# Performance work log

Hardware: AMD Instinct MI355X
Metric: run time of the kernel (lower is better)

## Reference

```python
import jax, jax.numpy as jnp
import numpy as np

E = 8          # num_experts
K = 2          # top_k
TEMP = 1.0     # router_temp
D = 1024       # model dim
H = 4 * D      # expert hidden dim
B, T = 2, 2048


def setup_inputs() -> dict:
    key = jax.random.key(0)
    ks = jax.random.split(key, 5)
    x = jax.random.normal(ks[0], (B, T, D), jnp.float32)
    gate_w = jax.random.normal(ks[1], (D, E), jnp.float32) * 0.02
    gate_b = jnp.zeros((E,), jnp.float32)
    w1 = jax.random.normal(ks[2], (E, D, H), jnp.float32) * 0.02
    b1 = jnp.zeros((E, H), jnp.float32)
    w2 = jax.random.normal(ks[3], (E, H, D), jnp.float32) * 0.02
    b2 = jnp.zeros((E, D), jnp.float32)
    return {"x": x, "gate_w": gate_w, "gate_b": gate_b,
            "w1": w1, "b1": b1, "w2": w2, "b2": b2}


def reference(x, gate_w, gate_b, w1, b1, w2, b2):
    b, t, d = x.shape
    xf = x.reshape(-1, d)                                    # [N, D]
    logits = xf @ gate_w + gate_b                            # [N, E]
    gates = jax.nn.softmax(logits / TEMP, axis=-1)
    topk_gates, topk_idx = jax.lax.top_k(gates, K)           # [N, K]
    topk_gates = topk_gates / (topk_gates.sum(-1, keepdims=True) + 1e-9)
    # combine weight per (token, expert): sum over k slots routed to expert e
    comb = (jax.nn.one_hot(topk_idx, E, dtype=xf.dtype)
            * topk_gates[..., None]).sum(axis=1)             # [N, E]
    out = jnp.zeros_like(xf)
    for e in range(E):  # small fixed loop over experts
        h = jax.nn.gelu(xf @ w1[e] + b1[e], approximate=False)  # exact GELU (torch default)
        out = out + comb[:, e:e + 1] * (h @ w2[e] + b2[e])
    return out.reshape(b, t, d)
```

## Files before the change

kernel.cpp:

```cpp
#include <hip/hip_runtime.h>
#include <math.h>

#define NTOK 4096
#define DIM  1024
#define HID  4096
#define NEXP 8
#define NROW 8192
#define KSPLIT 2

typedef __bf16 bf16;
typedef __attribute__((ext_vector_type(8))) __bf16 bf16x8;
typedef __attribute__((ext_vector_type(4))) float floatx4;

__device__ __forceinline__ void gl_lds16(const bf16* g, bf16* l) {
    __builtin_amdgcn_global_load_lds(
        (const __attribute__((address_space(1))) void*)g,
        (__attribute__((address_space(3))) void*)l, 16, 0, 0);
}

__device__ __forceinline__ float gelu_f(float v) {
    float x  = v * 0.70710678118654752f;
    float ax = fabsf(x);
    float t  = __builtin_amdgcn_rcpf(fmaf(0.3275911f, ax, 1.0f));
    float p  = fmaf(fmaf(fmaf(fmaf(1.061405429f, t, -1.453152027f),
                              t, 1.421413741f),
                         t, -0.284496736f),
                    t, 0.254829592f);
    p *= t;
    float ex = __expf(-x * x);
    float er = fmaf(-p, ex, 1.0f);
    er = copysignf(er, v);
    return 0.5f * v * (1.0f + er);
}

__global__ void zero_k(int* __restrict__ p) {
    if (threadIdx.x < 16) p[threadIdx.x] = 0;
}

__global__ __launch_bounds__(256) void router_k(
    const float* __restrict__ x, const float* __restrict__ gw, const float* __restrict__ gb,
    int* __restrict__ counts, int* __restrict__ tok_e, float* __restrict__ tok_g,
    bf16* __restrict__ xb)
{
    __shared__ float gws[NEXP][DIM];
    int t = threadIdx.x;
#pragma unroll
    for (int i = 0; i < 32; ++i) {
        int g = i * 256 + t;
        gws[g & 7][g >> 3] = gw[g];
    }
    __syncthreads();

    int gid = blockIdx.x * 256 + t;
    int wv = gid >> 6, lane = gid & 63;
    const float* xr = x + (size_t)wv * DIM;
    bf16* xw = xb + (size_t)wv * DIM;
    float acc[NEXP];
#pragma unroll
    for (int e = 0; e < NEXP; ++e) acc[e] = 0.f;
#pragma unroll
    for (int j = 0; j < 16; ++j) {
        int d = lane + j * 64;
        float xv = xr[d];
        xw[d] = (bf16)xv;
#pragma unroll
        for (int e = 0; e < NEXP; ++e) acc[e] += xv * gws[e][d];
    }
#pragma unroll
    for (int off = 32; off > 0; off >>= 1) {
#pragma unroll
        for (int e = 0; e < NEXP; ++e) acc[e] += __shfl_xor(acc[e], off, 64);
    }
    if (lane == 0) {
        float lg[NEXP], m = -1e30f;
        for (int e = 0; e < NEXP; ++e) { lg[e] = acc[e] + gb[e]; m = fmaxf(m, lg[e]); }
        float p[NEXP], s = 0.f;
        for (int e = 0; e < NEXP; ++e) { p[e] = expf(lg[e] - m); s += p[e]; }
        int e0 = 0;
        for (int e = 1; e < NEXP; ++e) if (p[e] > p[e0]) e0 = e;
        int e1 = (e0 == 0) ? 1 : 0;
        for (int e = 0; e < NEXP; ++e) if (e != e0 && p[e] > p[e1]) e1 = e;
        float g0 = p[e0] / s, g1 = p[e1] / s;
        float gs = g0 + g1 + 1e-9f;
        g0 /= gs; g1 /= gs;
        tok_e[wv * 2] = e0; tok_e[wv * 2 + 1] = e1;
        tok_g[wv * 2] = g0; tok_g[wv * 2 + 1] = g1;
        atomicAdd(&counts[e0], 1);
        atomicAdd(&counts[e1], 1);
    }
}

__global__ void scan_k(const int* __restrict__ counts, int* __restrict__ base)
{
    if (threadIdx.x == 0) {
        int s = 0;
#pragma unroll
        for (int e = 0; e < NEXP; ++e) { base[e] = s; s += counts[e]; }
        base[NEXP] = s;
    }
}

__global__ __launch_bounds__(256) void scatter_k(
    const int* __restrict__ tok_e, const float* __restrict__ tok_g,
    const int* __restrict__ base, int* __restrict__ counts2,
    int* __restrict__ row_token, float* __restrict__ row_gate, int* __restrict__ tok_row)
{
    int tk = blockIdx.x * 256 + threadIdx.x;
    if (tk >= NTOK) return;
#pragma unroll
    for (int k = 0; k < 2; ++k) {
        int e = tok_e[tk * 2 + k];
        int slot = atomicAdd(&counts2[e], 1);
        int r = base[e] + slot;
        row_token[r] = tk;
        row_gate[r] = tok_g[tk * 2 + k];
        tok_row[tk * 2 + k] = r;
    }
}

__global__ __launch_bounds__(256) void transpose_k(
    const float* __restrict__ src, bf16* __restrict__ dst,
    int R, int sld, size_t soff, size_t es, size_t ed)
{
    int e = blockIdx.z;
    bf16* d = dst + (size_t)e * ed;
    __shared__ __align__(16) bf16 tile[64 * 64];
    int t = threadIdx.x;
    int r0 = blockIdx.y * 64, c0 = blockIdx.x * 64;
#pragma unroll
    for (int i = 0; i < 2; ++i) {
        int c = t + i * 256;
        int rr = c >> 3, cc = c & 7;
        size_t eo = soff + (size_t)e * es + (size_t)(r0 + rr) * sld + c0 + cc * 8;
        floatx4 a = *(const floatx4*)(src + eo);
        floatx4 b = *(const floatx4*)(src + eo + 4);
        bf16x8 v;
#pragma unroll
        for (int j = 0; j < 4; ++j) { v[j] = (bf16)a[j]; v[4 + j] = (bf16)b[j]; }
        *(bf16x8*)&tile[rr * 64 + ((cc ^ ((rr >> 3) & 7)) * 8)] = v;
    }
    __syncthreads();
#pragma unroll
    for (int i = 0; i < 2; ++i) {
        int c = t + i * 256;
        int oc = c >> 3;
        int occ = c & 7;
        bf16x8 v;
#pragma unroll
        for (int j = 0; j < 8; ++j) {
            int r = occ * 8 + j;
            int p = (oc >> 3) ^ ((r >> 3) & 7);
            v[j] = tile[r * 64 + p * 8 + (oc & 7)];
        }
        *(bf16x8*)&d[(size_t)(c0 + oc) * R + r0 + occ * 8] = v;
    }
}

__global__ __launch_bounds__(256) void gemm1_k(
    const bf16* __restrict__ xb, const bf16* __restrict__ w1t, const float* __restrict__ b1,
    const int* __restrict__ counts, const int* __restrict__ base,
    const int* __restrict__ row_token, bf16* __restrict__ hbuf, int Nc, int bias_off)
{
    const int e = blockIdx.z;
    const int cnt = counts[e];
    const int rt = blockIdx.y;
    if (rt * 128 >= cnt) return;
    const int rb = base[e] + rt * 128;
    const int rend = base[e] + cnt;
    const int n0 = blockIdx.x * 128;

    __shared__ __align__(16) bf16 As[2][128 * 32];
    __shared__ __align__(16) bf16 Bs[2][128 * 32];

    const int t = threadIdx.x;
    const int wv = t >> 6, lane = t & 63;
    const int s0 = t, s1 = t + 256;
    const int ar0 = s0 >> 2, ac0 = (s0 & 3) ^ ((s0 >> 3) & 3);
    const int ar1 = s1 >> 2, ac1 = (s1 & 3) ^ ((s1 >> 3) & 3);
    int rr0 = rb + ar0; if (rr0 > NROW - 1) rr0 = NROW - 1;
    int rr1 = rb + ar1; if (rr1 > NROW - 1) rr1 = NROW - 1;
    const bf16* ga0 = xb + (size_t)row_token[rr0] * DIM + ac0 * 8;
    const bf16* ga1 = xb + (size_t)row_token[rr1] * DIM + ac1 * 8;
    const bf16* wb = w1t + (size_t)e * Nc * DIM;
    const bf16* gb0 = wb + (size_t)(n0 + ar0) * DIM + ac0 * 8;
    const bf16* gb1 = wb + (size_t)(n0 + ar1) * DIM + ac1 * 8;
    const int off0 = wv * 512, off1 = 2048 + wv * 512;

    floatx4 acc[4][4];
#pragma unroll
    for (int i = 0; i < 4; ++i)
#pragma unroll
        for (int j = 0; j < 4; ++j) acc[i][j] = floatx4{0.f, 0.f, 0.f, 0.f};

    const int wr = (wv >> 1) * 64, wc = (wv & 1) * 64;
    const int lr = lane & 15;
    const int ck = lane >> 4;

    gl_lds16(ga0, &As[0][off0]); gl_lds16(ga1, &As[0][off1]);
    gl_lds16(gb0, &Bs[0][off0]); gl_lds16(gb1, &Bs[0][off1]);

    const int NSTEP = DIM / 32;
#pragma unroll 2
    for (int i = 0; i < NSTEP; ++i) {
        const int bc = i & 1;
        asm volatile("s_waitcnt vmcnt(0)" ::: "memory");
        __builtin_amdgcn_s_barrier();
        asm volatile("" ::: "memory");
        if (i + 1 < NSTEP) {
            const int kn = (i + 1) * 32;
            gl_lds16(ga0 + kn, &As[bc ^ 1][off0]); gl_lds16(ga1 + kn, &As[bc ^ 1][off1]);
            gl_lds16(gb0 + kn, &Bs[bc ^ 1][off0]); gl_lds16(gb1 + kn, &Bs[bc ^ 1][off1]);
        }
        bf16x8 af[4], bg[4];
#pragma unroll
        for (int q = 0; q < 4; ++q) {
            int r = wr + q * 16 + lr;
            af[q] = *(const bf16x8*)&As[bc][r * 32 + ((ck ^ ((r >> 1) & 3)) * 8)];
        }
#pragma unroll
        for (int q = 0; q < 4; ++q) {
            int r = wc + q * 16 + lr;
            bg[q] = *(const bf16x8*)&Bs[bc][r * 32 + ((ck ^ ((r >> 1) & 3)) * 8)];
        }
        __builtin_amdgcn_s_setprio(1);
#pragma unroll
        for (int mi = 0; mi < 4; ++mi)
#pragma unroll
            for (int ni = 0; ni < 4; ++ni)
                acc[mi][ni] = __builtin_amdgcn_mfma_f32_16x16x32_bf16(af[mi], bg[ni], acc[mi][ni], 0, 0, 0);
        __builtin_amdgcn_s_setprio(0);
    }

#pragma unroll
    for (int mi = 0; mi < 4; ++mi) {
#pragma unroll
        for (int r = 0; r < 4; ++r) {
            int m = wr + mi * 16 + (lane >> 4) * 4 + r;
            int gr = rb + m;
            if (gr < rend) {
#pragma unroll
                for (int ni = 0; ni < 4; ++ni) {
                    int col = n0 + wc + ni * 16 + lr;
                    float v = acc[mi][ni][r] + b1[e * HID + bias_off + col];
                    hbuf[(size_t)gr * Nc + col] = (bf16)gelu_f(v);
                }
            }
        }
    }
}

__global__ __launch_bounds__(256) void gemm2_k(
    const bf16* __restrict__ hbuf, const bf16* __restrict__ w2t,
    const int* __restrict__ counts, const int* __restrict__ base,
    float* __restrict__ ybuf, int Kc, int first)
{
    const int e  = blockIdx.z >> 1;
    const int ks = blockIdx.z & 1;
    const int cnt = counts[e];
    const int rt = blockIdx.y;
    if (rt * 128 >= cnt) return;
    const int rb = base[e] + rt * 128;
    const int rend = base[e] + cnt;
    const int n0 = blockIdx.x * 128;
    const int klen = Kc / KSPLIT;
    const int kbeg = ks * klen;

    __shared__ __align__(16) bf16 As[3][128 * 32];
    __shared__ __align__(16) bf16 Bs[3][128 * 32];

    const int t = threadIdx.x;
    const int wv = t >> 6, lane = t & 63;
    const int s0 = t, s1 = t + 256;
    const int ar0 = s0 >> 2, ac0 = (s0 & 3) ^ ((s0 >> 3) & 3);
    const int ar1 = s1 >> 2, ac1 = (s1 & 3) ^ ((s1 >> 3) & 3);
    int rr0 = rb + ar0; if (rr0 > NROW - 1) rr0 = NROW - 1;
    int rr1 = rb + ar1; if (rr1 > NROW - 1) rr1 = NROW - 1;
    const bf16* ga0 = hbuf + (size_t)rr0 * Kc + kbeg + ac0 * 8;
    const bf16* ga1 = hbuf + (size_t)rr1 * Kc + kbeg + ac1 * 8;
    const bf16* wb = w2t + (size_t)e * DIM * Kc;
    const bf16* gb0 = wb + (size_t)(n0 + ar0) * Kc + kbeg + ac0 * 8;
    const bf16* gb1 = wb + (size_t)(n0 + ar1) * Kc + kbeg + ac1 * 8;
    const int off0 = wv * 512, off1 = 2048 + wv * 512;

    floatx4 acc[4][4];
#pragma unroll
    for (int i = 0; i < 4; ++i)
#pragma unroll
        for (int j = 0; j < 4; ++j) acc[i][j] = floatx4{0.f, 0.f, 0.f, 0.f};

    const int wr = (wv >> 1) * 64, wc = (wv & 1) * 64;
    const int lr = lane & 15;
    const int ck = lane >> 4;

    gl_lds16(ga0,      &As[0][off0]); gl_lds16(ga1,      &As[0][off1]);
    gl_lds16(gb0,      &Bs[0][off0]); gl_lds16(gb1,      &Bs[0][off1]);
    gl_lds16(ga0 + 32, &As[1][off0]); gl_lds16(ga1 + 32, &As[1][off1]);
    gl_lds16(gb0 + 32, &Bs[1][off0]); gl_lds16(gb1 + 32, &Bs[1][off1]);

    const int nstep = klen >> 5;
    int bc = 0;
    for (int i = 0; i < nstep; ++i) {
        if (i + 1 < nstep) asm volatile("s_waitcnt vmcnt(4)" ::: "memory");
        else               asm volatile("s_waitcnt vmcnt(0)" ::: "memory");
        __builtin_amdgcn_s_barrier();
        asm volatile("" ::: "memory");
        if (i + 2 < nstep) {
            int bs = bc + 2; if (bs >= 3) bs -= 3;
            const int kn = (i + 2) * 32;
            gl_lds16(ga0 + kn, &As[bs][off0]); gl_lds16(ga1 + kn, &As[bs][off1]);
            gl_lds16(gb0 + kn, &Bs[bs][off0]); gl_lds16(gb1 + kn, &Bs[bs][off1]);
        }
        bf16x8 af[4], bg[4];
#pragma unroll
        for (int q = 0; q < 4; ++q) {
            int r = wr + q * 16 + lr;
            af[q] = *(const bf16x8*)&As[bc][r * 32 + ((ck ^ ((r >> 1) & 3)) * 8)];
        }
#pragma unroll
        for (int q = 0; q < 4; ++q) {
            int r = wc + q * 16 + lr;
            bg[q] = *(const bf16x8*)&Bs[bc][r * 32 + ((ck ^ ((r >> 1) & 3)) * 8)];
        }
        __builtin_amdgcn_s_setprio(1);
#pragma unroll
        for (int mi = 0; mi < 4; ++mi)
#pragma unroll
            for (int ni = 0; ni < 4; ++ni)
                acc[mi][ni] = __builtin_amdgcn_mfma_f32_16x16x32_bf16(af[mi], bg[ni], acc[mi][ni], 0, 0, 0);
        __builtin_amdgcn_s_setprio(0);
        bc += 1; if (bc >= 3) bc -= 3;
    }

    float* yb = ybuf + (size_t)ks * NROW * DIM;
#pragma unroll
    for (int mi = 0; mi < 4; ++mi) {
#pragma unroll
        for (int r = 0; r < 4; ++r) {
            int m = wr + mi * 16 + (lane >> 4) * 4 + r;
            int gr = rb + m;
            if (gr < rend) {
#pragma unroll
                for (int ni = 0; ni < 4; ++ni) {
                    int col = n0 + wc + ni * 16 + lr;
                    size_t idx = (size_t)gr * DIM + col;
                    float v = acc[mi][ni][r];
                    yb[idx] = first ? v : (yb[idx] + v);
                }
            }
        }
    }
}

__global__ __launch_bounds__(256) void combine_k(
    const float* __restrict__ ybuf, const int* __restrict__ tok_row,
    const int* __restrict__ tok_e, const float* __restrict__ tok_g,
    const float* __restrict__ b2, float* __restrict__ out)
{
    int i = blockIdx.x * 256 + threadIdx.x;
    int tk = i >> 8;
    int dc = (i & 255) * 4;
    int ra = tok_row[tk * 2], rbx = tok_row[tk * 2 + 1];
    int ea = tok_e[tk * 2],  eb = tok_e[tk * 2 + 1];
    float ga = tok_g[tk * 2], gbv = tok_g[tk * 2 + 1];
    const float* y0 = ybuf;
    const float* y1 = ybuf + (size_t)NROW * DIM;
    floatx4 a0 = *(const floatx4*)&y0[(size_t)ra * DIM + dc];
    floatx4 a1 = *(const floatx4*)&y1[(size_t)ra * DIM + dc];
    floatx4 b0 = *(const floatx4*)&y0[(size_t)rbx * DIM + dc];
    floatx4 b1v = *(const floatx4*)&y1[(size_t)rbx * DIM + dc];
    floatx4 b2a = *(const floatx4*)&b2[ea * DIM + dc];
    floatx4 b2b = *(const floatx4*)&b2[eb * DIM + dc];
    floatx4 o;
#pragma unroll
    for (int j = 0; j < 4; ++j)
        o[j] = ga * (a0[j] + a1[j] + b2a[j]) + gbv * (b0[j] + b1v[j] + b2b[j]);
    *(floatx4*)&out[(size_t)tk * DIM + dc] = o;
}

extern "C" void kernel_launch(void* const* d_in, const int* in_sizes, int n_in,
                              void* d_out, int out_size, void* d_ws, size_t ws_size,
                              hipStream_t stream)
{
    const float* x  = (const float*)d_in[0];
    const float* gw = (const float*)d_in[1];
    const float* gb = (const float*)d_in[2];
    const float* w1 = (const float*)d_in[3];
    const float* b1 = (const float*)d_in[4];
    const float* w2 = (const float*)d_in[5];
    const float* b2 = (const float*)d_in[6];
    float* out = (float*)d_out;

    char* w = (char*)d_ws;
    int*   counts  = (int*)(w + 0);
    int*   counts2 = (int*)(w + 32);
    int*   base    = (int*)(w + 64);
    int*   tok_e   = (int*)(w + 256);
    float* tok_g   = (float*)(w + 256 + 32768);
    int*   row_tok = (int*)(w + 256 + 2 * 32768);
    float* row_g   = (float*)(w + 256 + 3 * 32768);
    int*   tok_row = (int*)(w + 256 + 4 * 32768);
    size_t off = 256 + 5 * 32768;
    bf16*  xb   = (bf16*)(w + off);   off += (size_t)NTOK * DIM * 2;
    float* ybuf = (float*)(w + off);  off += (size_t)KSPLIT * NROW * DIM * 4;

    int Hc = HID;
    for (;;) {
        size_t need = off + (size_t)NEXP * Hc * DIM * 2 + (size_t)NROW * Hc * 2;
        if (need <= ws_size || Hc == 128) break;
        Hc >>= 1;
    }
    bf16* wT   = (bf16*)(w + off);  off += (size_t)NEXP * Hc * DIM * 2;
    bf16* hbuf = (bf16*)(w + off);

    zero_k<<<1, 64, 0, stream>>>(counts);
    router_k<<<NTOK / 4, 256, 0, stream>>>(x, gw, gb, counts, tok_e, tok_g, xb);
    scan_k<<<1, 64, 0, stream>>>(counts, base);
    scatter_k<<<NTOK / 256, 256, 0, stream>>>(tok_e, tok_g, base, counts2, row_tok, row_g, tok_row);

    const int nc = HID / Hc;
    for (int ch = 0; ch < nc; ++ch) {
        transpose_k<<<dim3(Hc / 64, DIM / 64, NEXP), 256, 0, stream>>>(
            w1, wT, DIM, HID, (size_t)ch * Hc, (size_t)DIM * HID, (size_t)Hc * DIM);
        gemm1_k<<<dim3(Hc / 128, 32, NEXP), 256, 0, stream>>>(
            xb, wT, b1, counts, base, row_tok, hbuf, Hc, ch * Hc);
        transpose_k<<<dim3(DIM / 64, Hc / 64, NEXP), 256, 0, stream>>>(
            w2, wT, Hc, DIM, (size_t)ch * Hc * DIM, (size_t)HID * DIM, (size_t)DIM * Hc);
        gemm2_k<<<dim3(DIM / 128, 32, NEXP * KSPLIT), 256, 0, stream>>>(
            hbuf, wT, counts, base, ybuf, Hc, ch == 0);
    }

    combine_k<<<NTOK, 256, 0, stream>>>(ybuf, tok_row, tok_e, tok_g, b2, out);
}
```

Measured before the change: 694.2 us.

## Launch compact per-expert tile lists with XCD-aware block swizzle in GEMMs

The scan kernel now builds a compact list of (expert, row-tile) pairs, and both expert GEMMs launch a 1D grid sized to the maximum possible tile count. Before, the 3D grid spawned many blocks that exited at once for unused row tiles. Block indices are also remapped so that consecutive logical tiles land on the same XCD, which is meant to improve L2 reuse of expert weights and activations. The gemm1 index decode assumes 32 column tiles, so it relies on the full hidden chunk being used.

```diff
diff --git a/kernel.cpp b/kernel.cpp
--- a/kernel.cpp
+++ b/kernel.cpp
@@ -7,6 +7,7 @@
 #define NEXP 8
 #define NROW 8192
 #define KSPLIT 2
+#define MAXTILE 71
 
 typedef __bf16 bf16;
 typedef __attribute__((ext_vector_type(8))) __bf16 bf16x8;
@@ -16,6 +17,11 @@
     __builtin_amdgcn_global_load_lds(
         (const __attribute__((address_space(1))) void*)g,
         (__attribute__((address_space(3))) void*)l, 16, 0, 0);
+}
+
+__device__ __forceinline__ int xcd_swz(int orig, int nwg) {
+    int q = nwg >> 3;
+    return (orig & 7) * q + (orig >> 3);
 }
 
 __device__ __forceinline__ float gelu_f(float v) {
@@ -90,13 +96,22 @@
     }
 }
 
-__global__ void scan_k(const int* __restrict__ counts, int* __restrict__ base)
+__global__ void scan_k(const int* __restrict__ counts, int* __restrict__ base,
+                       int* __restrict__ tile_e, int* __restrict__ tile_rt,
+                       int* __restrict__ ntile)
 {
     if (threadIdx.x == 0) {
-        int s = 0;
-#pragma unroll
-        for (int e = 0; e < NEXP; ++e) { base[e] = s; s += counts[e]; }
+        int s = 0, nt = 0;
+#pragma unroll
+        for (int e = 0; e < NEXP; ++e) {
+            base[e] = s;
+            int c = counts[e];
+            int nte = (c + 127) >> 7;
+            for (int rt = 0; rt < nte; ++rt) { tile_e[nt] = e; tile_rt[nt] = rt; ++nt; }
+            s += c;
+        }
         base[NEXP] = s;
+        ntile[0] = nt;
     }
 }
 
@@ -159,15 +174,17 @@
 __global__ __launch_bounds__(256) void gemm1_k(
     const bf16* __restrict__ xb, const bf16* __restrict__ w1t, const float* __restrict__ b1,
     const int* __restrict__ counts, const int* __restrict__ base,
+    const int* __restrict__ tile_e, const int* __restrict__ tile_rt,
+    const int* __restrict__ ntile,
     const int* __restrict__ row_token, bf16* __restrict__ hbuf, int Nc, int bias_off)
 {
-    const int e = blockIdx.z;
-    const int cnt = counts[e];
-    const int rt = blockIdx.y;
-    if (rt * 128 >= cnt) return;
-    const int rb = base[e] + rt * 128;
-    const int rend = base[e] + cnt;
-    const int n0 = blockIdx.x * 128;
+    const int lid = xcd_swz(blockIdx.x, gridDim.x);
+    const int ty = lid >> 5, tx = lid & 31;
+    if (ty >= ntile[0]) return;
+    const int e = tile_e[ty];
+    const int rb = base[e] + tile_rt[ty] * 128;
+    const int rend = base[e] + counts[e];
+    const int n0 = tx * 128;
 
     __shared__ __align__(16) bf16 As[2][128 * 32];
     __shared__ __align__(16) bf16 Bs[2][128 * 32];
@@ -252,16 +269,20 @@
 __global__ __launch_bounds__(256) void gemm2_k(
     const bf16* __restrict__ hbuf, const bf16* __restrict__ w2t,
     const int* __restrict__ counts, const int* __restrict__ base,
+    const int* __restrict__ tile_e, const int* __restrict__ tile_rt,
+    const int* __restrict__ ntile,
     float* __restrict__ ybuf, int Kc, int first)
 {
-    const int e  = blockIdx.z >> 1;
-    const int ks = blockIdx.z & 1;
-    const int cnt = counts[e];
-    const int rt = blockIdx.y;
-    if (rt * 128 >= cnt) return;
-    const int rb = base[e] + rt * 128;
-    const int rend = base[e] + cnt;
-    const int n0 = blockIdx.x * 128;
+    const int lid = xcd_swz(blockIdx.x, gridDim.x);
+    const int tx = lid & 7;
+    const int tmp = lid >> 3;
+    const int ks = tmp / MAXTILE;
+    const int ty = tmp - ks * MAXTILE;
+    if (ty >= ntile[0]) return;
+    const int e = tile_e[ty];
+    const int rb = base[e] + tile_rt[ty] * 128;
+    const int rend = base[e] + counts[e];
+    const int n0 = tx * 128;
     const int klen = Kc / KSPLIT;
     const int kbeg = ks * klen;
 
@@ -394,12 +415,15 @@
     int*   counts  = (int*)(w + 0);
     int*   counts2 = (int*)(w + 32);
     int*   base    = (int*)(w + 64);
-    int*   tok_e   = (int*)(w + 256);
-    float* tok_g   = (float*)(w + 256 + 32768);
-    int*   row_tok = (int*)(w + 256 + 2 * 32768);
-    float* row_g   = (float*)(w + 256 + 3 * 32768);
-    int*   tok_row = (int*)(w + 256 + 4 * 32768);
-    size_t off = 256 + 5 * 32768;
+    int*   ntile   = (int*)(w + 112);
+    int*   tile_e  = (int*)(w + 128);
+    int*   tile_rt = (int*)(w + 512);
+    int*   tok_e   = (int*)(w + 1024);
+    float* tok_g   = (float*)(w + 1024 + 32768);
+    int*   row_tok = (int*)(w + 1024 + 2 * 32768);
+    float* row_g   = (float*)(w + 1024 + 3 * 32768);
+    int*   tok_row = (int*)(w + 1024 + 4 * 32768);
+    size_t off = 1024 + 5 * 32768;
     bf16*  xb   = (bf16*)(w + off);   off += (size_t)NTOK * DIM * 2;
     float* ybuf = (float*)(w + off);  off += (size_t)KSPLIT * NROW * DIM * 4;
 
@@ -414,19 +438,19 @@
 
     zero_k<<<1, 64, 0, stream>>>(counts);
     router_k<<<NTOK / 4, 256, 0, stream>>>(x, gw, gb, counts, tok_e, tok_g, xb);
-    scan_k<<<1, 64, 0, stream>>>(counts, base);
+    scan_k<<<1, 64, 0, stream>>>(counts, base, tile_e, tile_rt, ntile);
     scatter_k<<<NTOK / 256, 256, 0, stream>>>(tok_e, tok_g, base, counts2, row_tok, row_g, tok_row);
 
     const int nc = HID / Hc;
     for (int ch = 0; ch < nc; ++ch) {
         transpose_k<<<dim3(Hc / 64, DIM / 64, NEXP), 256, 0, stream>>>(
             w1, wT, DIM, HID, (size_t)ch * Hc, (size_t)DIM * HID, (size_t)Hc * DIM);
-        gemm1_k<<<dim3(Hc / 128, 32, NEXP), 256, 0, stream>>>(
-            xb, wT, b1, counts, base, row_tok, hbuf, Hc, ch * Hc);
+        gemm1_k<<<MAXTILE * (Hc / 128), 256, 0, stream>>>(
+            xb, wT, b1, counts, base, tile_e, tile_rt, ntile, row_tok, hbuf, Hc, ch * Hc);
         transpose_k<<<dim3(DIM / 64, Hc / 64, NEXP), 256, 0, stream>>>(
             w2, wT, Hc, DIM, (size_t)ch * Hc * DIM, (size_t)HID * DIM, (size_t)DIM * Hc);
-        gemm2_k<<<dim3(DIM / 128, 32, NEXP * KSPLIT), 256, 0, stream>>>(
-            hbuf, wT, counts, base, ybuf, Hc, ch == 0);
+        gemm2_k<<<MAXTILE * KSPLIT * (DIM / 128), 256, 0, stream>>>(
+            hbuf, wT, counts, base, tile_e, tile_rt, ntile, ybuf, Hc, ch == 0);
     }
 
     combine_k<<<NTOK, 256, 0, stream>>>(ybuf, tok_row, tok_e, tok_g, b2, out);
```

Result: no change. 695.6 us (+0.2%).
